# Kernel optimization log

Hardware: AMD Instinct MI355X
Metric: run time of the kernel (lower is better)

The kernel has to match this reference:

```python
import jax, jax.numpy as jnp
import numpy as np

N_NODES = 10000
N_EDGES = 640000
D = 128            # node_dims == edge_dims
HID = 2 * D        # ff hidden
EPS = 1e-6


def _layernorm(x, g, b):
    mu = jnp.mean(x, axis=-1, keepdims=True)
    var = jnp.var(x, axis=-1, keepdims=True)
    return (x - mu) * jax.lax.rsqrt(var + EPS) * g + b


def setup_inputs() -> dict:
    key = jax.random.key(0)
    ks = jax.random.split(key, 16)
    def lin(k, fan_in, fan_out):
        lim = 1.0 / np.sqrt(fan_in)
        kw, kb = jax.random.split(k)
        W = jax.random.uniform(kw, (fan_in, fan_out), jnp.float32, -lim, lim)
        b = jax.random.uniform(kb, (fan_out,), jnp.float32, -lim, lim)
        return W, b
    x = jax.random.normal(ks[0], (N_NODES, D), jnp.float32)
    edge_index = jax.random.randint(ks[1], (2, N_EDGES), 0, N_NODES, jnp.int64)
    edge_attr = jax.random.normal(ks[2], (N_EDGES, D), jnp.float32)
    # message MLP: Linear(3D->D), ReLU, Linear(D->D), ReLU, Linear(D->D)
    W1, b1 = lin(ks[3], 3 * D, D)
    W2, b2 = lin(ks[4], D, D)
    W3, b3 = lin(ks[5], D, D)
    # feedforward: Linear(D->2D), ReLU, Linear(2D->D)
    F1, bf1 = lin(ks[6], D, HID)
    F2, bf2 = lin(ks[7], HID, D)
    g0 = jnp.ones((D,), jnp.float32); be0 = jnp.zeros((D,), jnp.float32)
    g1 = jnp.ones((D,), jnp.float32); be1 = jnp.zeros((D,), jnp.float32)
    return {"x": x, "edge_index": edge_index, "edge_attr": edge_attr,
            "W1": W1, "b1": b1, "W2": W2, "b2": b2, "W3": W3, "b3": b3,
            "F1": F1, "bf1": bf1, "F2": F2, "bf2": bf2,
            "g0": g0, "be0": be0, "g1": g1, "be1": be1}


def reference(x, edge_index, edge_attr, W1, b1, W2, b2, W3, b3,
              F1, bf1, F2, bf2, g0, be0, g1, be1):
    src = edge_index[0]  # j
    dst = edge_index[1]  # i
    # message: cat([h_V_i, edge_attr, h_V_j]) -> MLP  (E x 3D gather)
    m = jnp.concatenate([x[dst], edge_attr, x[src]], axis=-1)
    m = jax.nn.relu(m @ W1 + b1)
    m = jax.nn.relu(m @ W2 + b2)
    m = m @ W3 + b3  # [E, D]
    # scatter-mean over destination nodes
    sums = jax.ops.segment_sum(m, dst, num_segments=N_NODES)
    cnt = jax.ops.segment_sum(jnp.ones((N_EDGES,), m.dtype), dst, num_segments=N_NODES)
    dh = sums / jnp.maximum(cnt, 1.0)[:, None]
    # residual + norm (dropout is identity at inference)
    h = _layernorm(x + dh, g0, be0)
    # pointwise feedforward
    ff = jax.nn.relu(h @ F1 + bf1) @ F2 + bf2
    return _layernorm(h + ff, g1, be1)
```

## Files before the change

kernel.cpp:

```cpp
#include <hip/hip_runtime.h>


#define NE 640000
#define NN 10000
#define DD 128
#define HIDN 256
#define EPSF 1e-6f
#define TILES 20
#define EBLK 250

typedef __attribute__((ext_vector_type(8))) short short8;
typedef __attribute__((ext_vector_type(4))) float f32x4;

__device__ __forceinline__ unsigned short f2bf(float f) {
    union { float f; unsigned int u; } v; v.f = f;
    unsigned int r = v.u + 0x7FFFu + ((v.u >> 16) & 1u);
    return (unsigned short)(r >> 16);
}
__device__ __forceinline__ float bf2f(unsigned short h) {
    union { unsigned int u; float f; } v; v.u = ((unsigned int)h) << 16;
    return v.f;
}
__device__ __forceinline__ int swzcol(int row, int col) {
    return (((col >> 3) ^ (row & 7)) << 3) | (col & 7);
}
__device__ __forceinline__ const short8* frag(const unsigned short* buf,
                                              int row, int kc, int q) {
    int g = (kc * 4 + q) ^ (row & 7);
    return (const short8*)(buf + row * 128 + g * 8);
}

__global__ void prep_weights(const float* __restrict__ W1,
                             const float* __restrict__ W2,
                             const float* __restrict__ W3,
                             unsigned short* __restrict__ WT)
{
    int g = blockIdx.x * 256 + threadIdx.x;
    int layer = g >> 14, r = g & 16383;
    int n = r >> 7, k = r & 127;
    const float* W = (layer == 0) ? (W1 + 128 * DD) : (layer == 1 ? W2 : W3);
    WT[layer * 16384 + n * 128 + swzcol(n, k)] = f2bf(W[k * DD + n]);
}

__global__ __launch_bounds__(256)
void pq_kernel(const float* __restrict__ x, const float* __restrict__ W1,
               const float* __restrict__ b1,
               unsigned short* __restrict__ Pb, unsigned short* __restrict__ Qb)
{
    __shared__ float sx[16][DD];
    const int t = threadIdx.x;
    const int nb = blockIdx.x * 16;

#pragma unroll
    for (int p = 0; p < 2; ++p) {
        int f = t + p * 256;
        int row = f >> 5, c4 = (f & 31) << 2;
        *(float4*)&sx[row][c4] = *(const float4*)(x + (long)(nb + row) * DD + c4);
    }
    __syncthreads();

    const int j  = t & 127;
    const int g8 = (t >> 7) << 3;

    for (int pass = 0; pass < 2; ++pass) {
        const float* W = W1 + (pass ? 256 * DD : 0);
        float acc[8];
#pragma unroll
        for (int v = 0; v < 8; ++v) acc[v] = 0.f;
        for (int k4 = 0; k4 < DD; k4 += 4) {
            float w0 = W[(k4 + 0) * DD + j];
            float w1 = W[(k4 + 1) * DD + j];
            float w2 = W[(k4 + 2) * DD + j];
            float w3 = W[(k4 + 3) * DD + j];
#pragma unroll
            for (int v = 0; v < 8; ++v) {
                float4 hv = *(const float4*)&sx[g8 + v][k4];
                acc[v] = fmaf(hv.x, w0, acc[v]);
                acc[v] = fmaf(hv.y, w1, acc[v]);
                acc[v] = fmaf(hv.z, w2, acc[v]);
                acc[v] = fmaf(hv.w, w3, acc[v]);
            }
        }
        unsigned short* Out = pass ? Qb : Pb;
        float bb = pass ? 0.f : b1[j];
#pragma unroll
        for (int v = 0; v < 8; ++v)
            Out[(long)(nb + g8 + v) * DD + j] = f2bf(acc[v] + bb);
    }
}

__global__ __launch_bounds__(256, 1)
void edge_mfma(const float* __restrict__ ea, const int* __restrict__ ei,
               const unsigned short* __restrict__ WT,
               const unsigned short* __restrict__ Pb,
               const unsigned short* __restrict__ Qb,
               const float* __restrict__ b2, const float* __restrict__ b3,
               float* __restrict__ sums, float* __restrict__ cnt)
{
    __shared__ unsigned short sW[3 * 128 * 128];
    __shared__ unsigned short sA[4][32 * 128];

    const int t = threadIdx.x;
    const int wave = t >> 6, lane = t & 63;
    const int ln = lane & 15, q = lane >> 4;
    const int r0g = wave * 32;
    unsigned short* myA = sA[wave];

    {
        const uint4* s = (const uint4*)WT;
        uint4* d = (uint4*)sW;
#pragma unroll
        for (int p = 0; p < 24; ++p) d[t + p * 256] = s[t + p * 256];
    }
    __syncthreads();

    int rowoff[8];
#pragma unroll
    for (int r = 0; r < 8; ++r) rowoff[r] = (r >> 2) * 16 + q * 4 + (r & 3);

    float bv2[8], bv3[8];
#pragma unroll
    for (int ct = 0; ct < 8; ++ct) { bv2[ct] = b2[ct * 16 + ln]; bv3[ct] = b3[ct * 16 + ln]; }

    const long tb0 = (long)blockIdx.x * TILES * 128;

    float4 Aq[16];
    int dstR[8], srcR[8];
#pragma unroll
    for (int jj = 0; jj < 16; ++jj) {
        int f = lane + jj * 64;
        int srow = f >> 5, c4 = (f & 31) << 2;
        Aq[jj] = *(const float4*)(ea + (tb0 + r0g + srow) * DD + c4);
    }
#pragma unroll
    for (int r = 0; r < 8; ++r) {
        dstR[r] = ei[(long)NE + tb0 + r0g + rowoff[r]];
        srcR[r] = ei[tb0 + r0g + rowoff[r]];
    }

    for (int it = 0; it < TILES; ++it) {
        const long nb_ = tb0 + (long)((it + 1 < TILES) ? it + 1 : it) * 128;

        unsigned short pU[64], qU[64];
#pragma unroll
        for (int r = 0; r < 8; ++r) {
            long dof = (long)dstR[r] * DD, sof = (long)srcR[r] * DD;
#pragma unroll
            for (int ct = 0; ct < 8; ++ct) {
                pU[r * 8 + ct] = Pb[dof + ct * 16 + ln];
                qU[r * 8 + ct] = Qb[sof + ct * 16 + ln];
            }
        }

#pragma unroll
        for (int jj = 0; jj < 16; ++jj) {
            int f = lane + jj * 64;
            int srow = f >> 5, c4 = (f & 31) << 2;
            float4 v = Aq[jj];
            uint2 pk;
            pk.x = (unsigned)f2bf(v.x) | ((unsigned)f2bf(v.y) << 16);
            pk.y = (unsigned)f2bf(v.z) | ((unsigned)f2bf(v.w) << 16);
            *(uint2*)(myA + srow * 128 + swzcol(srow, c4)) = pk;
        }
        __builtin_amdgcn_wave_barrier();

        f32x4 acc[2][8];
#pragma unroll
        for (int rt = 0; rt < 2; ++rt)
#pragma unroll
            for (int ct = 0; ct < 8; ++ct)
#pragma unroll
                for (int rg = 0; rg < 4; ++rg)
                    acc[rt][ct][rg] = bf2f(pU[(rt * 4 + rg) * 8 + ct]) +
                                      bf2f(qU[(rt * 4 + rg) * 8 + ct]);

#pragma unroll
        for (int jj = 0; jj < 16; ++jj) {
            int f = lane + jj * 64;
            int srow = f >> 5, c4 = (f & 31) << 2;
            Aq[jj] = *(const float4*)(ea + (nb_ + r0g + srow) * DD + c4);
        }
        int ndst[8], nsrc[8];
#pragma unroll
        for (int r = 0; r < 8; ++r) {
            ndst[r] = ei[(long)NE + nb_ + r0g + rowoff[r]];
            nsrc[r] = ei[nb_ + r0g + rowoff[r]];
        }

#pragma unroll
        for (int kc = 0; kc < 4; ++kc) {
            short8 a0 = *frag(myA, ln, kc, q);
            short8 a1 = *frag(myA, 16 + ln, kc, q);
#pragma unroll
            for (int ct = 0; ct < 8; ++ct) {
                short8 b = *frag(sW, ct * 16 + ln, kc, q);
                acc[0][ct] = __builtin_amdgcn_mfma_f32_16x16x32_bf16(a0, b, acc[0][ct], 0, 0, 0);
                acc[1][ct] = __builtin_amdgcn_mfma_f32_16x16x32_bf16(a1, b, acc[1][ct], 0, 0, 0);
            }
        }
        __builtin_amdgcn_wave_barrier();
#pragma unroll
        for (int rt = 0; rt < 2; ++rt)
#pragma unroll
            for (int rg = 0; rg < 4; ++rg) {
                int row = rt * 16 + q * 4 + rg;
#pragma unroll
                for (int ct = 0; ct < 8; ++ct) {
                    int col = ct * 16 + ln;
                    myA[row * 128 + swzcol(row, col)] =
                        f2bf(fmaxf(acc[rt][ct][rg], 0.f));
                }
            }
        __builtin_amdgcn_wave_barrier();

#pragma unroll
        for (int rt = 0; rt < 2; ++rt)
#pragma unroll
            for (int ct = 0; ct < 8; ++ct) acc[rt][ct] = (f32x4)(0.f);
#pragma unroll
        for (int kc = 0; kc < 4; ++kc) {
            short8 a0 = *frag(myA, ln, kc, q);
            short8 a1 = *frag(myA, 16 + ln, kc, q);
#pragma unroll
            for (int ct = 0; ct < 8; ++ct) {
                short8 b = *frag(sW + 16384, ct * 16 + ln, kc, q);
                acc[0][ct] = __builtin_amdgcn_mfma_f32_16x16x32_bf16(a0, b, acc[0][ct], 0, 0, 0);
                acc[1][ct] = __builtin_amdgcn_mfma_f32_16x16x32_bf16(a1, b, acc[1][ct], 0, 0, 0);
            }
        }
        __builtin_amdgcn_wave_barrier();
#pragma unroll
        for (int rt = 0; rt < 2; ++rt)
#pragma unroll
            for (int rg = 0; rg < 4; ++rg) {
                int row = rt * 16 + q * 4 + rg;
#pragma unroll
                for (int ct = 0; ct < 8; ++ct) {
                    int col = ct * 16 + ln;
                    myA[row * 128 + swzcol(row, col)] =
                        f2bf(fmaxf(acc[rt][ct][rg] + bv2[ct], 0.f));
                }
            }
        __builtin_amdgcn_wave_barrier();

#pragma unroll
        for (int rt = 0; rt < 2; ++rt)
#pragma unroll
            for (int ct = 0; ct < 8; ++ct) acc[rt][ct] = (f32x4)(0.f);
#pragma unroll
        for (int kc = 0; kc < 4; ++kc) {
            short8 a0 = *frag(myA, ln, kc, q);
            short8 a1 = *frag(myA, 16 + ln, kc, q);
#pragma unroll
            for (int ct = 0; ct < 8; ++ct) {
                short8 b = *frag(sW + 2 * 16384, ct * 16 + ln, kc, q);
                acc[0][ct] = __builtin_amdgcn_mfma_f32_16x16x32_bf16(a0, b, acc[0][ct], 0, 0, 0);
                acc[1][ct] = __builtin_amdgcn_mfma_f32_16x16x32_bf16(a1, b, acc[1][ct], 0, 0, 0);
            }
        }
#pragma unroll
        for (int rt = 0; rt < 2; ++rt)
#pragma unroll
            for (int rg = 0; rg < 4; ++rg) {
                long dof = (long)dstR[rt * 4 + rg] * DD;
#pragma unroll
                for (int ct = 0; ct < 8; ++ct)
                    atomicAdd(sums + dof + ct * 16 + ln,
                              acc[rt][ct][rg] + bv3[ct]);
            }
        if (ln == 0) {
#pragma unroll
            for (int r = 0; r < 8; ++r) atomicAdd(cnt + dstR[r], 1.0f);
        }
#pragma unroll
        for (int r = 0; r < 8; ++r) { dstR[r] = ndst[r]; srcR[r] = nsrc[r]; }
    }
}

__global__ __launch_bounds__(256)
void node_fused(const float* __restrict__ x,
                const float* __restrict__ sums, const float* __restrict__ cnt,
                const float* __restrict__ F1, const float* __restrict__ bf1,
                const float* __restrict__ F2, const float* __restrict__ bf2,
                const float* __restrict__ g0, const float* __restrict__ be0,
                const float* __restrict__ g1, const float* __restrict__ be1,
                float* __restrict__ out)
{
    constexpr int NPB = 8;
    __shared__ float sh[NPB][DD];
    __shared__ float shid[NPB][HIDN];
    __shared__ float sz[NPB][DD];

    const int t = threadIdx.x;
    const int wave = t >> 6, lane = t & 63;
    const int half = lane >> 5, l2 = lane & 31;
    const int nl = wave * 2 + half;
    const int node = blockIdx.x * NPB + nl;
    const long base = (long)node * DD;

    float inv = 1.0f / fmaxf(cnt[node], 1.0f);
    float y[4], s = 0.f, ss = 0.f;
#pragma unroll
    for (int e = 0; e < 4; ++e) {
        int c = l2 + 32 * e;
        y[e] = x[base + c] + sums[base + c] * inv;
        s += y[e]; ss += y[e] * y[e];
    }
#pragma unroll
    for (int off = 16; off > 0; off >>= 1) {
        s += __shfl_down(s, off, 32); ss += __shfl_down(ss, off, 32);
    }
    s = __shfl(s, 0, 32); ss = __shfl(ss, 0, 32);
    float mean = s * (1.0f / DD);
    float var  = ss * (1.0f / DD) - mean * mean;
    float rstd = rsqrtf(var + EPSF);
#pragma unroll
    for (int e = 0; e < 4; ++e) {
        int c = l2 + 32 * e;
        sh[nl][c] = (y[e] - mean) * rstd * g0[c] + be0[c];
    }
    __syncthreads();

    float hacc[NPB];
    float bb = bf1[t];
#pragma unroll
    for (int v = 0; v < NPB; ++v) hacc[v] = bb;
    for (int k4 = 0; k4 < DD; k4 += 4) {
        float w0 = F1[(long)(k4 + 0) * HIDN + t];
        float w1 = F1[(long)(k4 + 1) * HIDN + t];
        float w2 = F1[(long)(k4 + 2) * HIDN + t];
        float w3 = F1[(long)(k4 + 3) * HIDN + t];
#pragma unroll
        for (int v = 0; v < NPB; ++v) {
            float4 hv = *(const float4*)&sh[v][k4];
            hacc[v] = fmaf(hv.x, w0, hacc[v]);
            hacc[v] = fmaf(hv.y, w1, hacc[v]);
            hacc[v] = fmaf(hv.z, w2, hacc[v]);
            hacc[v] = fmaf(hv.w, w3, hacc[v]);
        }
    }
#pragma unroll
    for (int v = 0; v < NPB; ++v) shid[v][t] = fmaxf(hacc[v], 0.f);
    __syncthreads();

    const int col = t & (DD - 1);
    const int grp = (t >> 7) * 4;
    float o[4];
#pragma unroll
    for (int v = 0; v < 4; ++v) o[v] = bf2[col];
    for (int k4 = 0; k4 < HIDN; k4 += 4) {
        float w0 = F2[(long)(k4 + 0) * DD + col];
        float w1 = F2[(long)(k4 + 1) * DD + col];
        float w2 = F2[(long)(k4 + 2) * DD + col];
        float w3 = F2[(long)(k4 + 3) * DD + col];
#pragma unroll
        for (int v = 0; v < 4; ++v) {
            float4 hv = *(const float4*)&shid[grp + v][k4];
            o[v] = fmaf(hv.x, w0, o[v]);
            o[v] = fmaf(hv.y, w1, o[v]);
            o[v] = fmaf(hv.z, w2, o[v]);
            o[v] = fmaf(hv.w, w3, o[v]);
        }
    }
#pragma unroll
    for (int v = 0; v < 4; ++v) sz[grp + v][col] = sh[grp + v][col] + o[v];
    __syncthreads();

    float z[4]; s = 0.f; ss = 0.f;
#pragma unroll
    for (int e = 0; e < 4; ++e) {
        int c = l2 + 32 * e;
        z[e] = sz[nl][c]; s += z[e]; ss += z[e] * z[e];
    }
#pragma unroll
    for (int off = 16; off > 0; off >>= 1) {
        s += __shfl_down(s, off, 32); ss += __shfl_down(ss, off, 32);
    }
    s = __shfl(s, 0, 32); ss = __shfl(ss, 0, 32);
    mean = s * (1.0f / DD);
    var  = ss * (1.0f / DD) - mean * mean;
    rstd = rsqrtf(var + EPSF);
#pragma unroll
    for (int e = 0; e < 4; ++e) {
        int c = l2 + 32 * e;
        out[base + c] = (z[e] - mean) * rstd * g1[c] + be1[c];
    }
}

extern "C" void kernel_launch(void* const* d_in, const int* in_sizes, int n_in,
                              void* d_out, int out_size, void* d_ws, size_t ws_size,
                              hipStream_t stream)
{
    const float* x   = (const float*)d_in[0];
    const int*   ei  = (const int*)  d_in[1];
    const float* ea  = (const float*)d_in[2];
    const float* W1  = (const float*)d_in[3];
    const float* b1  = (const float*)d_in[4];
    const float* W2  = (const float*)d_in[5];
    const float* b2  = (const float*)d_in[6];
    const float* W3  = (const float*)d_in[7];
    const float* b3  = (const float*)d_in[8];
    const float* F1  = (const float*)d_in[9];
    const float* bf1 = (const float*)d_in[10];
    const float* F2  = (const float*)d_in[11];
    const float* bf2 = (const float*)d_in[12];
    const float* g0  = (const float*)d_in[13];
    const float* be0 = (const float*)d_in[14];
    const float* g1  = (const float*)d_in[15];
    const float* be1 = (const float*)d_in[16];
    float* out = (float*)d_out;

    char* ws = (char*)d_ws;
    float*          sums = (float*)(ws);
    float*          cnt  = (float*)(ws + 5120000);
    unsigned short* WT   = (unsigned short*)(ws + 5160192);
    unsigned short* Pb   = (unsigned short*)(ws + 5258752);
    unsigned short* Qb   = (unsigned short*)(ws + 7818752);

    hipMemsetAsync(ws, 0, 5160000, stream);
    prep_weights<<<192, 256, 0, stream>>>(W1, W2, W3, WT);
    pq_kernel<<<NN / 16, 256, 0, stream>>>(x, W1, b1, Pb, Qb);
    edge_mfma<<<EBLK, 256, 0, stream>>>(ea, ei, WT, Pb, Qb, b2, b3, sums, cnt);
    node_fused<<<NN / 8, 256, 0, stream>>>(x, sums, cnt, F1, bf1, F2, bf2,
                                           g0, be0, g1, be1, out);
}
```

Measured before the change: 874.9 us.

## Merge prep kernels, permute P/Q layout, register-fed first MFMA, 512-thread edge blocks

Merges weight preparation and the P/Q projection into one launch. Stores P/Q in a permuted column order so each lane fetches its eight needed bf16 values with one 16-byte load instead of eight scalar gathers. Loads edge_attr directly in MFMA A-fragment order and converts it in registers, which skips the LDS staging round-trip for the first layer. Edge blocks grow to 8 waves sharing the weight LDS copy, with 10 tiles per block; register pressure under launch_bounds(512,2) may rise.

Result: faster. 807.9 us (-7.7%).

```diff
diff --git a/kernel.cpp b/kernel.cpp
--- a/kernel.cpp
+++ b/kernel.cpp
@@ -6,8 +6,8 @@
 #define DD 128
 #define HIDN 256
 #define EPSF 1e-6f
-#define TILES 20
-#define EBLK 250
+#define TILES4 10
+#define EBLK4 250
 
 typedef __attribute__((ext_vector_type(8))) short short8;
 typedef __attribute__((ext_vector_type(4))) float f32x4;
@@ -30,26 +30,24 @@
     return (const short8*)(buf + row * 128 + g * 8);
 }
 
-__global__ void prep_weights(const float* __restrict__ W1,
-                             const float* __restrict__ W2,
-                             const float* __restrict__ W3,
-                             unsigned short* __restrict__ WT)
+__global__ __launch_bounds__(256)
+void prep_pq(const float* __restrict__ W1, const float* __restrict__ W2,
+             const float* __restrict__ W3, const float* __restrict__ b1,
+             const float* __restrict__ x,
+             unsigned short* __restrict__ WT,
+             unsigned short* __restrict__ Pp, unsigned short* __restrict__ Qp)
 {
-    int g = blockIdx.x * 256 + threadIdx.x;
-    int layer = g >> 14, r = g & 16383;
-    int n = r >> 7, k = r & 127;
-    const float* W = (layer == 0) ? (W1 + 128 * DD) : (layer == 1 ? W2 : W3);
-    WT[layer * 16384 + n * 128 + swzcol(n, k)] = f2bf(W[k * DD + n]);
-}
-
-__global__ __launch_bounds__(256)
-void pq_kernel(const float* __restrict__ x, const float* __restrict__ W1,
-               const float* __restrict__ b1,
-               unsigned short* __restrict__ Pb, unsigned short* __restrict__ Qb)
-{
+    const int t = threadIdx.x;
+    if (blockIdx.x < 192) {
+        int g = blockIdx.x * 256 + t;
+        int layer = g >> 14, r = g & 16383;
+        int n = r >> 7, k = r & 127;
+        const float* W = (layer == 0) ? (W1 + 128 * DD) : (layer == 1 ? W2 : W3);
+        WT[layer * 16384 + n * 128 + swzcol(n, k)] = f2bf(W[k * DD + n]);
+        return;
+    }
     __shared__ float sx[16][DD];
-    const int t = threadIdx.x;
-    const int nb = blockIdx.x * 16;
+    const int nb = (blockIdx.x - 192) * 16;
 
 #pragma unroll
     for (int p = 0; p < 2; ++p) {
@@ -61,6 +59,7 @@
 
     const int j  = t & 127;
     const int g8 = (t >> 7) << 3;
+    const int pj = ((j & 15) << 3) + (j >> 4);
 
     for (int pass = 0; pass < 2; ++pass) {
         const float* W = W1 + (pass ? 256 * DD : 0);
@@ -81,124 +80,119 @@
                 acc[v] = fmaf(hv.w, w3, acc[v]);
             }
         }
-        unsigned short* Out = pass ? Qb : Pb;
+        unsigned short* Out = pass ? Qp : Pp;
         float bb = pass ? 0.f : b1[j];
 #pragma unroll
         for (int v = 0; v < 8; ++v)
-            Out[(long)(nb + g8 + v) * DD + j] = f2bf(acc[v] + bb);
-    }
-}
-
-__global__ __launch_bounds__(256, 1)
+            Out[(long)(nb + g8 + v) * 128 + pj] = f2bf(acc[v] + bb);
+    }
+}
+
+__global__ __launch_bounds__(512, 2)
 void edge_mfma(const float* __restrict__ ea, const int* __restrict__ ei,
                const unsigned short* __restrict__ WT,
-               const unsigned short* __restrict__ Pb,
-               const unsigned short* __restrict__ Qb,
+               const unsigned short* __restrict__ Pp,
+               const unsigned short* __restrict__ Qp,
                const float* __restrict__ b2, const float* __restrict__ b3,
                float* __restrict__ sums, float* __restrict__ cnt)
 {
-    __shared__ unsigned short sW[3 * 128 * 128];
-    __shared__ unsigned short sA[4][32 * 128];
+    __shared__ unsigned short sW[3 * 16384];
+    __shared__ unsigned short sAct[8 * 4096];
 
     const int t = threadIdx.x;
     const int wave = t >> 6, lane = t & 63;
     const int ln = lane & 15, q = lane >> 4;
-    const int r0g = wave * 32;
-    unsigned short* myA = sA[wave];
+    unsigned short* myA = sAct + wave * 4096;
 
     {
         const uint4* s = (const uint4*)WT;
         uint4* d = (uint4*)sW;
 #pragma unroll
-        for (int p = 0; p < 24; ++p) d[t + p * 256] = s[t + p * 256];
+        for (int p = 0; p < 12; ++p) d[t + p * 512] = s[t + p * 512];
     }
     __syncthreads();
 
-    int rowoff[8];
-#pragma unroll
-    for (int r = 0; r < 8; ++r) rowoff[r] = (r >> 2) * 16 + q * 4 + (r & 3);
-
     float bv2[8], bv3[8];
 #pragma unroll
-    for (int ct = 0; ct < 8; ++ct) { bv2[ct] = b2[ct * 16 + ln]; bv3[ct] = b3[ct * 16 + ln]; }
-
-    const long tb0 = (long)blockIdx.x * TILES * 128;
+    for (int ct = 0; ct < 8; ++ct) {
+        bv2[ct] = b2[ct * 16 + ln];
+        bv3[ct] = b3[ct * 16 + ln];
+    }
+
+    const long blkbase = (long)blockIdx.x * (TILES4 * 256);
 
     float4 Aq[16];
     int dstR[8], srcR[8];
-#pragma unroll
-    for (int jj = 0; jj < 16; ++jj) {
-        int f = lane + jj * 64;
-        int srow = f >> 5, c4 = (f & 31) << 2;
-        Aq[jj] = *(const float4*)(ea + (tb0 + r0g + srow) * DD + c4);
-    }
-#pragma unroll
-    for (int r = 0; r < 8; ++r) {
-        dstR[r] = ei[(long)NE + tb0 + r0g + rowoff[r]];
-        srcR[r] = ei[tb0 + r0g + rowoff[r]];
-    }
-
-    for (int it = 0; it < TILES; ++it) {
-        const long nb_ = tb0 + (long)((it + 1 < TILES) ? it + 1 : it) * 128;
-
-        unsigned short pU[64], qU[64];
+    {
+        long tb = blkbase;
+#pragma unroll
+        for (int rt = 0; rt < 2; ++rt)
+#pragma unroll
+            for (int kc = 0; kc < 4; ++kc) {
+                long row = tb + wave * 32 + rt * 16 + ln;
+                const float* p = ea + row * DD + kc * 32 + q * 8;
+                Aq[rt * 8 + kc * 2 + 0] = *(const float4*)(p);
+                Aq[rt * 8 + kc * 2 + 1] = *(const float4*)(p + 4);
+            }
 #pragma unroll
         for (int r = 0; r < 8; ++r) {
-            long dof = (long)dstR[r] * DD, sof = (long)srcR[r] * DD;
-#pragma unroll
-            for (int ct = 0; ct < 8; ++ct) {
-                pU[r * 8 + ct] = Pb[dof + ct * 16 + ln];
-                qU[r * 8 + ct] = Qb[sof + ct * 16 + ln];
-            }
-        }
-
-#pragma unroll
-        for (int jj = 0; jj < 16; ++jj) {
-            int f = lane + jj * 64;
-            int srow = f >> 5, c4 = (f & 31) << 2;
-            float4 v = Aq[jj];
-            uint2 pk;
-            pk.x = (unsigned)f2bf(v.x) | ((unsigned)f2bf(v.y) << 16);
-            pk.y = (unsigned)f2bf(v.z) | ((unsigned)f2bf(v.w) << 16);
-            *(uint2*)(myA + srow * 128 + swzcol(srow, c4)) = pk;
-        }
-        __builtin_amdgcn_wave_barrier();
+            long row = tb + wave * 32 + (r >> 2) * 16 + q * 4 + (r & 3);
+            dstR[r] = ei[(long)NE + row];
+            srcR[r] = ei[row];
+        }
+    }
+
+    for (int it = 0; it < TILES4; ++it) {
+        short8 af[2][4];
+#pragma unroll
+        for (int rt = 0; rt < 2; ++rt)
+#pragma unroll
+            for (int kc = 0; kc < 4; ++kc) {
+                const float* f0 = (const float*)&Aq[rt * 8 + kc * 2];
+                short8 v;
+#pragma unroll
+                for (int jj = 0; jj < 8; ++jj) v[jj] = (short)f2bf(f0[jj]);
+                af[rt][kc] = v;
+            }
 
         f32x4 acc[2][8];
 #pragma unroll
-        for (int rt = 0; rt < 2; ++rt)
+        for (int r = 0; r < 8; ++r) {
+            uint4 pv = *(const uint4*)(Pp + (long)dstR[r] * 128 + ln * 8);
+            uint4 qv = *(const uint4*)(Qp + (long)srcR[r] * 128 + ln * 8);
+            const unsigned short* pe = (const unsigned short*)&pv;
+            const unsigned short* qe = (const unsigned short*)&qv;
 #pragma unroll
             for (int ct = 0; ct < 8; ++ct)
-#pragma unroll
-                for (int rg = 0; rg < 4; ++rg)
-                    acc[rt][ct][rg] = bf2f(pU[(rt * 4 + rg) * 8 + ct]) +
-                                      bf2f(qU[(rt * 4 + rg) * 8 + ct]);
-
-#pragma unroll
-        for (int jj = 0; jj < 16; ++jj) {
-            int f = lane + jj * 64;
-            int srow = f >> 5, c4 = (f & 31) << 2;
-            Aq[jj] = *(const float4*)(ea + (nb_ + r0g + srow) * DD + c4);
-        }
+                acc[r >> 2][ct][r & 3] = bf2f(pe[ct]) + bf2f(qe[ct]);
+        }
+
+        long nb_ = blkbase + (long)((it + 1 < TILES4) ? it + 1 : it) * 256;
         int ndst[8], nsrc[8];
 #pragma unroll
+        for (int rt = 0; rt < 2; ++rt)
+#pragma unroll
+            for (int kc = 0; kc < 4; ++kc) {
+                long row = nb_ + wave * 32 + rt * 16 + ln;
+                const float* p = ea + row * DD + kc * 32 + q * 8;
+                Aq[rt * 8 + kc * 2 + 0] = *(const float4*)(p);
+                Aq[rt * 8 + kc * 2 + 1] = *(const float4*)(p + 4);
+            }
+#pragma unroll
         for (int r = 0; r < 8; ++r) {
-            ndst[r] = ei[(long)NE + nb_ + r0g + rowoff[r]];
-            nsrc[r] = ei[nb_ + r0g + rowoff[r]];
-        }
-
-#pragma unroll
-        for (int kc = 0; kc < 4; ++kc) {
-            short8 a0 = *frag(myA, ln, kc, q);
-            short8 a1 = *frag(myA, 16 + ln, kc, q);
+            long row = nb_ + wave * 32 + (r >> 2) * 16 + q * 4 + (r & 3);
+            ndst[r] = ei[(long)NE + row];
+            nsrc[r] = ei[row];
+        }
+
+#pragma unroll
+        for (int kc = 0; kc < 4; ++kc)
 #pragma unroll
             for (int ct = 0; ct < 8; ++ct) {
                 short8 b = *frag(sW, ct * 16 + ln, kc, q);
-                acc[0][ct] = __builtin_amdgcn_mfma_f32_16x16x32_bf16(a0, b, acc[0][ct], 0, 0, 0);
-                acc[1][ct] = __builtin_amdgcn_mfma_f32_16x16x32_bf16(a1, b, acc[1][ct], 0, 0, 0);
-            }
-        }
-        __builtin_amdgcn_wave_barrier();
+                acc[0][ct] = __builtin_amdgcn_mfma_f32_16x16x32_bf16(af[0][kc], b, acc[0][ct], 0, 0, 0);
+                acc[1][ct] = __builtin_amdgcn_mfma_f32_16x16x32_bf16(af[1][kc], b, acc[1][ct], 0, 0, 0);
+            }
 #pragma unroll
         for (int rt = 0; rt < 2; ++rt)
 #pragma unroll
@@ -253,7 +247,7 @@
             short8 a1 = *frag(myA, 16 + ln, kc, q);
 #pragma unroll
             for (int ct = 0; ct < 8; ++ct) {
-                short8 b = *frag(sW + 2 * 16384, ct * 16 + ln, kc, q);
+                short8 b = *frag(sW + 32768, ct * 16 + ln, kc, q);
                 acc[0][ct] = __builtin_amdgcn_mfma_f32_16x16x32_bf16(a0, b, acc[0][ct], 0, 0, 0);
                 acc[1][ct] = __builtin_amdgcn_mfma_f32_16x16x32_bf16(a1, b, acc[1][ct], 0, 0, 0);
             }
@@ -414,13 +408,12 @@
     float*          sums = (float*)(ws);
     float*          cnt  = (float*)(ws + 5120000);
     unsigned short* WT   = (unsigned short*)(ws + 5160192);
-    unsigned short* Pb   = (unsigned short*)(ws + 5258752);
-    unsigned short* Qb   = (unsigned short*)(ws + 7818752);
+    unsigned short* Pp   = (unsigned short*)(ws + 5258752);
+    unsigned short* Qp   = (unsigned short*)(ws + 7818752);
 
     hipMemsetAsync(ws, 0, 5160000, stream);
-    prep_weights<<<192, 256, 0, stream>>>(W1, W2, W3, WT);
-    pq_kernel<<<NN / 16, 256, 0, stream>>>(x, W1, b1, Pb, Qb);
-    edge_mfma<<<EBLK, 256, 0, stream>>>(ea, ei, WT, Pb, Qb, b2, b3, sums, cnt);
+    prep_pq<<<192 + NN / 16, 256, 0, stream>>>(W1, W2, W3, b1, x, WT, Pp, Qp);
+    edge_mfma<<<EBLK4, 512, 0, stream>>>(ea, ei, WT, Pp, Qp, b2, b3, sums, cnt);
     node_fused<<<NN / 8, 256, 0, stream>>>(x, sums, cnt, F1, bf1, F2, bf2,
                                            g0, be0, g1, be1, out);
 }
```
